# Kernel optimization log

Hardware: AMD Instinct MI355X
Metric: run time of the kernel (lower is better)

Reference implementation:

```python
import jax, jax.numpy as jnp
import numpy as np


def fps(xyz, nsamples):
    # xyz: [B, N, 3] -> [B, nsamples] furthest-point-sample indices (int32)
    def single(p):
        N = p.shape[0]
        def step(carry, _):
            dists, last = carry
            d = jnp.sum((p - p[last]) ** 2, axis=-1)
            dists = jnp.minimum(dists, d)
            return (dists, jnp.argmax(dists).astype(jnp.int32)), last
        init = (jnp.full((N,), 1e10, p.dtype), jnp.int32(0))
        _, idx = jax.lax.scan(step, init, None, length=nsamples)
        return idx
    return jax.vmap(single)(xyz)


def bn_relu(x, g, b, m, v):
    # inference BatchNorm2d folded into scale/shift, then ReLU; x: [B,C,S,N]
    s = g * jax.lax.rsqrt(v + 1e-5)
    return jax.nn.relu(x * s[None, :, None, None] + (b - m * s)[None, :, None, None])


def setup_inputs() -> dict:
    key = jax.random.key(0)
    ks = jax.random.split(key, 6)
    B, N, C, S = 8, 16384, 64, 5
    return dict(
        fg_xyz=jax.random.normal(ks[0], (B, N, 3), jnp.float32),
        fg_features=jax.random.normal(ks[1], (B, C, N), jnp.float32),
        bg_xyz=jax.random.normal(ks[2], (B, N, 3), jnp.float32),
        bg_features=jax.random.normal(ks[3], (B, C, N), jnp.float32),
        w1=jax.random.normal(ks[4], (C, 2 * C), jnp.float32) * (1.0 / np.sqrt(2 * C)),
        g1=jnp.ones((C,), jnp.float32), b1=jnp.zeros((C,), jnp.float32),
        m1=jnp.zeros((C,), jnp.float32), v1=jnp.ones((C,), jnp.float32),
        w2=jax.random.normal(ks[5], (C, C), jnp.float32) * (1.0 / np.sqrt(C)),
        g2=jnp.ones((C,), jnp.float32), b2=jnp.zeros((C,), jnp.float32),
        m2=jnp.zeros((C,), jnp.float32), v2=jnp.ones((C,), jnp.float32),
        nsamples=5,
    )


def reference(fg_xyz, fg_features, bg_xyz, bg_features,
              w1, g1, b1, m1, v1, w2, g2, b2, m2, v2, nsamples):
    B, C, N = fg_features.shape
    S = nsamples
    # D-FPS sample S background points, gather their features: [B, C, S]
    idx = fps(bg_xyz, S)
    sample_bg = jnp.take_along_axis(
        bg_features, jnp.broadcast_to(idx[:, None, :], (B, C, S)), axis=2)
    fg_exp = fg_features[:, :, None, :]                           # [B, C, 1, N]
    # candidates = [fg itself, S sampled bg feats tiled over the N fg points]
    fused_origin = jnp.concatenate(
        [fg_exp, jnp.broadcast_to(sample_bg[:, :, :, None], (B, C, S, N))], axis=2)  # [B,C,S+1,N]
    # weight-net input: fg feature concatenated with each candidate along channels
    fusion_in = jnp.concatenate(
        [jnp.broadcast_to(fg_exp, (B, C, S + 1, N)), fused_origin], axis=1)          # [B,2C,S+1,N]
    h = bn_relu(jnp.einsum('oc,bcsn->bosn', w1, fusion_in), g1, b1, m1, v1)
    w = bn_relu(jnp.einsum('oc,bcsn->bosn', w2, h), g2, b2, m2, v2)                  # [B,C,S+1,N]
    final_feats = jnp.sum(w * fused_origin, axis=2, keepdims=True)                   # [B,C,1,N]
    return fg_xyz, final_feats
```

## Files before the change

kernel.cpp:

```cpp
#include <hip/hip_runtime.h>
#include <hip/hip_bf16.h>

#define B_ 8
#define N_ 16384
#define C_ 64
#define S_ 5

typedef float v4f __attribute__((ext_vector_type(4)));
typedef __bf16 v8bf __attribute__((ext_vector_type(8)));
typedef unsigned int v4u __attribute__((ext_vector_type(4)));

static __device__ __forceinline__ unsigned short f2bf(float f) {
    unsigned int u = __float_as_uint(f);
    u += 0x7fffu + ((u >> 16) & 1u);
    return (unsigned short)(u >> 16);
}
static __device__ __forceinline__ float bf2f(unsigned short s) {
    return __uint_as_float(((unsigned int)s) << 16);
}

#define GETF(A, i) (((i) & 3) == 0 ? A[(i) >> 2].x : ((i) & 3) == 1 ? A[(i) >> 2].y \
                    : ((i) & 3) == 2 ? A[(i) >> 2].z : A[(i) >> 2].w)

__global__ __launch_bounds__(1024, 4) void prep_all(
    const float* __restrict__ bg_xyz, const float* __restrict__ bg_feat,
    const float* __restrict__ w1, const float* __restrict__ g1, const float* __restrict__ b1,
    const float* __restrict__ m1, const float* __restrict__ v1,
    const float* __restrict__ w2, const float* __restrict__ g2, const float* __restrict__ b2,
    const float* __restrict__ m2, const float* __restrict__ v2,
    const float* __restrict__ fg_xyz, float* __restrict__ out_xyz,
    float* __restrict__ bb1, float* __restrict__ bb2,
    unsigned short* __restrict__ wa_bf, unsigned short* __restrict__ wc_bf,
    unsigned short* __restrict__ w2_bf,
    float* __restrict__ sbg, float* __restrict__ ebb) {
    const int blk = blockIdx.x;
    const int t = threadIdx.x;

    if (blk >= 9) {
        const int i = (blk - 9) * 1024 + t;
        ((float4*)out_xyz)[i] = ((const float4*)fg_xyz)[i];
        return;
    }

    if (blk == 8) {
        for (int i = t; i < 64 * 64; i += 1024) {
            const int o = i >> 6, c = i & 63;
            const float s1 = g1[o] / sqrtf(v1[o] + 1e-5f);
            const float s2 = g2[o] / sqrtf(v2[o] + 1e-5f);
            const float a = s1 * w1[o * 128 + c];
            const float bbv = s1 * w1[o * 128 + 64 + c];
            wa_bf[o * 64 + c] = f2bf(a);
            wc_bf[o * 64 + c] = f2bf(a + bbv);
            w2_bf[o * 64 + c] = f2bf(s2 * w2[o * 64 + c]);
        }
        if (t < 64) {
            const float s1 = g1[t] / sqrtf(v1[t] + 1e-5f);
            const float s2 = g2[t] / sqrtf(v2[t] + 1e-5f);
            bb1[t] = b1[t] - m1[t] * s1;
            bb2[t] = b2[t] - m2[t] * s2;
        }
        return;
    }

    const int b = blk;
    const float* p = bg_xyz + (size_t)b * N_ * 3;

    float4 f4[12];
    {
        const float4* pv = (const float4*)p + t * 12;
#pragma unroll
        for (int i = 0; i < 12; ++i) f4[i] = pv[i];
    }
    float px[16], py[16], pz[16], dist[16];
#pragma unroll
    for (int k = 0; k < 16; ++k) {
        px[k] = GETF(f4, 3 * k);
        py[k] = GETF(f4, 3 * k + 1);
        pz[k] = GETF(f4, 3 * k + 2);
        dist[k] = 1e10f;
    }

    __shared__ float s_best[16];
    __shared__ int s_bidx[16];
    __shared__ int s_last;
    __shared__ int s_idx[S_];
    __shared__ float sf[S_][64];
    int last = 0;
    if (t == 0) s_idx[0] = 0;

    for (int step = 1; step < S_; ++step) {
        const float lx = p[last * 3 + 0];
        const float ly = p[last * 3 + 1];
        const float lz = p[last * 3 + 2];
        float best = -1.0f;
        int bidx = 0;
#pragma unroll
        for (int k = 0; k < 16; ++k) {
            float dx = px[k] - lx, dy = py[k] - ly, dz = pz[k] - lz;
            float d = dx * dx + dy * dy + dz * dz;
            float nd = fminf(dist[k], d);
            dist[k] = nd;
            if (nd > best) { best = nd; bidx = t * 16 + k; }
        }
#pragma unroll
        for (int off = 32; off > 0; off >>= 1) {
            float ob = __shfl_down(best, off, 64);
            int oi = __shfl_down(bidx, off, 64);
            if (ob > best || (ob == best && oi < bidx)) { best = ob; bidx = oi; }
        }
        if ((t & 63) == 0) { s_best[t >> 6] = best; s_bidx[t >> 6] = bidx; }
        __syncthreads();
        if (t == 0) {
            float bb = s_best[0];
            int bi = s_bidx[0];
#pragma unroll
            for (int w = 1; w < 16; ++w) {
                if (s_best[w] > bb || (s_best[w] == bb && s_bidx[w] < bi)) {
                    bb = s_best[w];
                    bi = s_bidx[w];
                }
            }
            s_last = bi;
            s_idx[step] = bi;
        }
        __syncthreads();
        last = s_last;
        __syncthreads();
    }

    __syncthreads();
    if (t < S_ * 64) {
        const int j = t >> 6, c = t & 63;
        sf[j][c] = bg_feat[(size_t)b * C_ * N_ + (size_t)c * N_ + s_idx[j]];
    }
    __syncthreads();
    if (t < S_ * 64) {
        const int j = t >> 6, o = t & 63;
        const float s1 = g1[o] * rsqrtf(v1[o] + 1e-5f);
        const float4* wr = (const float4*)&w1[o * 128 + 64];
        float acc = 0.f;
#pragma unroll
        for (int c4 = 0; c4 < 16; ++c4) {
            float4 wv = wr[c4];
            acc += wv.x * sf[j][c4 * 4 + 0] + wv.y * sf[j][c4 * 4 + 1] +
                   wv.z * sf[j][c4 * 4 + 2] + wv.w * sf[j][c4 * 4 + 3];
        }
        sbg[(b * S_ + j) * 64 + o] = sf[j][o];
        ebb[(b * S_ + j) * 64 + o] = s1 * acc + (b1[o] - m1[o] * s1);
    }
}

#define PITCH 72

__global__ __launch_bounds__(256, 4) void fusion_main(
    const float* __restrict__ fg_feat,
    const unsigned short* __restrict__ wa_bf, const unsigned short* __restrict__ wc_bf,
    const unsigned short* __restrict__ w2_bf,
    const float* __restrict__ bb1g, const float* __restrict__ bb2g,
    const float* __restrict__ ebbg, const float* __restrict__ sbgg,
    float* __restrict__ out) {
    __shared__ __align__(16) unsigned short Ft[2][64 * PITCH];
    __shared__ __align__(16) unsigned short Ht[64 * PITCH];
    __shared__ __align__(16) float cEbb[S_ * 64];
    __shared__ __align__(16) float cSbg[S_ * 64];
    __shared__ __align__(16) float cBb1[64];
    __shared__ __align__(16) float cBb2[64];

    const int t = threadIdx.x;
    const int b = blockIdx.y;
    const float* Fbase = fg_feat + (size_t)b * C_ * N_;
    const size_t outb = (size_t)b * C_ * N_;

    for (int i = t; i < S_ * 64; i += 256) {
        cEbb[i] = ebbg[b * (S_ * 64) + i];
        cSbg[i] = sbgg[b * (S_ * 64) + i];
    }
    if (t < 64) { cBb1[t] = bb1g[t]; cBb2[t] = bb2g[t]; }

    const int lane = t & 63;
    const int wv = t >> 6;
    const int o0 = wv * 16;
    const int m = lane & 15;
    const int q = lane >> 4;
    const int o4 = o0 + 4 * q;

    const int arow = o0 + m;
    v8bf aWa[2], aWc[2], aW2[2];
#pragma unroll
    for (int ks = 0; ks < 2; ++ks) {
        aWa[ks] = *(const v8bf*)&wa_bf[arow * 64 + ks * 32 + q * 8];
        aWc[ks] = *(const v8bf*)&wc_bf[arow * 64 + ks * 32 + q * 8];
        aW2[ks] = *(const v8bf*)&w2_bf[arow * 64 + ks * 32 + q * 8];
    }

    const int sn = t & 63;
    const int cg = (t >> 6) * 16;

    {
        const float* Fg = Fbase + (size_t)blockIdx.x * 64 + sn;
        float fr[16];
#pragma unroll
        for (int i = 0; i < 16; ++i) fr[i] = Fg[(size_t)(cg + i) * N_];
        v4u w0, w1v;
#pragma unroll
        for (int i = 0; i < 8; ++i) {
            unsigned int pk = (unsigned int)f2bf(fr[2 * i]) |
                              ((unsigned int)f2bf(fr[2 * i + 1]) << 16);
            if (i < 4) w0[i] = pk; else w1v[i - 4] = pk;
        }
        *(v4u*)&Ft[0][sn * PITCH + cg] = w0;
        *(v4u*)&Ft[0][sn * PITCH + cg + 8] = w1v;
    }
    __syncthreads();

    float fr1[16];
    {
        const float* Fg1 = Fbase + (size_t)(blockIdx.x + 128) * 64 + sn;
#pragma unroll
        for (int i = 0; i < 16; ++i) fr1[i] = Fg1[(size_t)(cg + i) * N_];
    }

    const v4f bb1r = *(const v4f*)&cBb1[o4];
    const v4f bb2r = *(const v4f*)&cBb2[o4];

    auto tile_compute = [&](const unsigned short* F, size_t obase) {
        v8bf bF[4][2];
#pragma unroll
        for (int nb = 0; nb < 4; ++nb)
#pragma unroll
            for (int ks = 0; ks < 2; ++ks)
                bF[nb][ks] = *(const v8bf*)&F[(nb * 16 + m) * PITCH + ks * 32 + q * 8];

        v4f U[4], U0[4];
#pragma unroll
        for (int nb = 0; nb < 4; ++nb) {
            v4f z = {0.f, 0.f, 0.f, 0.f};
            z = __builtin_amdgcn_mfma_f32_16x16x32_bf16(aWa[0], bF[nb][0], z, 0, 0, 0);
            U[nb] = __builtin_amdgcn_mfma_f32_16x16x32_bf16(aWa[1], bF[nb][1], z, 0, 0, 0);
            v4f z2 = {0.f, 0.f, 0.f, 0.f};
            z2 = __builtin_amdgcn_mfma_f32_16x16x32_bf16(aWc[0], bF[nb][0], z2, 0, 0, 0);
            U0[nb] = __builtin_amdgcn_mfma_f32_16x16x32_bf16(aWc[1], bF[nb][1], z2, 0, 0, 0);
        }

        v4f acc[4];
#pragma unroll
        for (int nb = 0; nb < 4; ++nb) acc[nb] = (v4f){0.f, 0.f, 0.f, 0.f};

#pragma unroll
        for (int s = 0; s < 6; ++s) {
            v4f cv = (s == 0) ? bb1r : *(const v4f*)&cEbb[(s - 1) * 64 + o4];
#pragma unroll
            for (int nb = 0; nb < 4; ++nb) {
                v4f u = (s == 0) ? U0[nb] : U[nb];
                float2 e01, e23;
                e01.x = fmaxf(u[0] + cv[0], 0.f);
                e01.y = fmaxf(u[1] + cv[1], 0.f);
                e23.x = fmaxf(u[2] + cv[2], 0.f);
                e23.y = fmaxf(u[3] + cv[3], 0.f);
                __hip_bfloat162 h01 = __float22bfloat162_rn(e01);
                __hip_bfloat162 h23 = __float22bfloat162_rn(e23);
                unsigned int lo, hi;
                __builtin_memcpy(&lo, &h01, 4);
                __builtin_memcpy(&hi, &h23, 4);
                unsigned long long vv = (unsigned long long)lo | ((unsigned long long)hi << 32);
                *(unsigned long long*)&Ht[(nb * 16 + m) * PITCH + o4] = vv;
            }
            __syncthreads();

            v4f p4[4];
#pragma unroll
            for (int nb = 0; nb < 4; ++nb) {
                v8bf h0 = *(const v8bf*)&Ht[(nb * 16 + m) * PITCH + q * 8];
                v8bf h1 = *(const v8bf*)&Ht[(nb * 16 + m) * PITCH + 32 + q * 8];
                v4f z = {0.f, 0.f, 0.f, 0.f};
                z = __builtin_amdgcn_mfma_f32_16x16x32_bf16(aW2[0], h0, z, 0, 0, 0);
                p4[nb] = __builtin_amdgcn_mfma_f32_16x16x32_bf16(aW2[1], h1, z, 0, 0, 0);
            }
            __syncthreads();

#pragma unroll
            for (int nb = 0; nb < 4; ++nb) {
                if (s == 0) {
                    unsigned long long fv =
                        *(const unsigned long long*)&F[(nb * 16 + m) * PITCH + o4];
#pragma unroll
                    for (int r = 0; r < 4; ++r) {
                        float wgt = fmaxf(p4[nb][r] + bb2r[r], 0.f);
                        acc[nb][r] += wgt * bf2f((unsigned short)(fv >> (16 * r)));
                    }
                } else {
                    const v4f sb = *(const v4f*)&cSbg[(s - 1) * 64 + o4];
#pragma unroll
                    for (int r = 0; r < 4; ++r) {
                        float wgt = fmaxf(p4[nb][r] + bb2r[r], 0.f);
                        acc[nb][r] += wgt * sb[r];
                    }
                }
            }
        }

#pragma unroll
        for (int nb = 0; nb < 4; ++nb)
#pragma unroll
            for (int r = 0; r < 4; ++r)
                out[obase + (size_t)(o4 + r) * N_ + (nb * 16 + m)] = acc[nb][r];
    };

    tile_compute(&Ft[0][0], outb + (size_t)blockIdx.x * 64);

    {
        v4u w0, w1v;
#pragma unroll
        for (int i = 0; i < 8; ++i) {
            unsigned int pk = (unsigned int)f2bf(fr1[2 * i]) |
                              ((unsigned int)f2bf(fr1[2 * i + 1]) << 16);
            if (i < 4) w0[i] = pk; else w1v[i - 4] = pk;
        }
        *(v4u*)&Ft[1][sn * PITCH + cg] = w0;
        *(v4u*)&Ft[1][sn * PITCH + cg + 8] = w1v;
    }
    __syncthreads();

    tile_compute(&Ft[1][0], outb + (size_t)(blockIdx.x + 128) * 64);
}

extern "C" void kernel_launch(void* const* d_in, const int* in_sizes, int n_in,
                              void* d_out, int out_size, void* d_ws, size_t ws_size,
                              hipStream_t stream) {
    const float* fg_xyz = (const float*)d_in[0];
    const float* fg_feat = (const float*)d_in[1];
    const float* bg_xyz = (const float*)d_in[2];
    const float* bg_feat = (const float*)d_in[3];
    const float* w1 = (const float*)d_in[4];
    const float* g1 = (const float*)d_in[5];
    const float* b1 = (const float*)d_in[6];
    const float* m1 = (const float*)d_in[7];
    const float* v1 = (const float*)d_in[8];
    const float* w2 = (const float*)d_in[9];
    const float* g2 = (const float*)d_in[10];
    const float* b2 = (const float*)d_in[11];
    const float* m2 = (const float*)d_in[12];
    const float* v2 = (const float*)d_in[13];

    float* ws = (float*)d_ws;
    float* ebb = ws;
    float* sbg = ebb + 2560;
    float* bb1 = sbg + 2560;
    float* bb2 = bb1 + 64;
    unsigned short* wa_bf = (unsigned short*)(bb2 + 64);
    unsigned short* wc_bf = wa_bf + 4096;
    unsigned short* w2_bf = wc_bf + 4096;

    float* out_feats = (float*)d_out + (size_t)B_ * N_ * 3;

    prep_all<<<105, 1024, 0, stream>>>(bg_xyz, bg_feat,
                                       w1, g1, b1, m1, v1, w2, g2, b2, m2, v2,
                                       fg_xyz, (float*)d_out,
                                       bb1, bb2, wa_bf, wc_bf, w2_bf, sbg, ebb);
    fusion_main<<<dim3(128, B_), 256, 0, stream>>>(
        fg_feat, wa_bf, wc_bf, w2_bf, bb1, bb2, ebb, sbg, out_feats);
}
```

Baseline: 198.0 us.

## Process one tile per block and double-buffer hidden tile to halve barriers

fusion_main now handles a single 64-point tile per block, launching twice as many blocks instead of looping over two tiles with a prefetched second tile. The hidden-activation LDS buffer is double-buffered by sample index, so the second barrier per sample step is gone and the W2 MFMA is fused with the accumulation. The change also drops the minimum-occupancy launch-bounds hints and cleans up the FPS point unpacking and bf16 packing. It removes half the syncthreads in the inner loop, but gives up the cross-tile global-load prefetch overlap.

```diff
diff --git a/kernel.cpp b/kernel.cpp
--- a/kernel.cpp
+++ b/kernel.cpp
@@ -18,11 +18,14 @@
 static __device__ __forceinline__ float bf2f(unsigned short s) {
     return __uint_as_float(((unsigned int)s) << 16);
 }
-
-#define GETF(A, i) (((i) & 3) == 0 ? A[(i) >> 2].x : ((i) & 3) == 1 ? A[(i) >> 2].y \
-                    : ((i) & 3) == 2 ? A[(i) >> 2].z : A[(i) >> 2].w)
-
-__global__ __launch_bounds__(1024, 4) void prep_all(
+static __device__ __forceinline__ unsigned int pk2bf(float a, float b) {
+    float2 f2; f2.x = a; f2.y = b;
+    __hip_bfloat162 h2 = __float22bfloat162_rn(f2);
+    unsigned int u; __builtin_memcpy(&u, &h2, 4);
+    return u;
+}
+
+__global__ __launch_bounds__(1024) void prep_all(
     const float* __restrict__ bg_xyz, const float* __restrict__ bg_feat,
     const float* __restrict__ w1, const float* __restrict__ g1, const float* __restrict__ b1,
     const float* __restrict__ m1, const float* __restrict__ v1,
@@ -65,19 +68,21 @@
     const int b = blk;
     const float* p = bg_xyz + (size_t)b * N_ * 3;
 
-    float4 f4[12];
+    float px[16], py[16], pz[16], dist[16];
     {
         const float4* pv = (const float4*)p + t * 12;
 #pragma unroll
-        for (int i = 0; i < 12; ++i) f4[i] = pv[i];
-    }
-    float px[16], py[16], pz[16], dist[16];
-#pragma unroll
-    for (int k = 0; k < 16; ++k) {
-        px[k] = GETF(f4, 3 * k);
-        py[k] = GETF(f4, 3 * k + 1);
-        pz[k] = GETF(f4, 3 * k + 2);
-        dist[k] = 1e10f;
+        for (int g = 0; g < 4; ++g) {
+            float4 a = pv[g * 3 + 0];
+            float4 bq = pv[g * 3 + 1];
+            float4 c = pv[g * 3 + 2];
+            px[g * 4 + 0] = a.x;  py[g * 4 + 0] = a.y;  pz[g * 4 + 0] = a.z;
+            px[g * 4 + 1] = a.w;  py[g * 4 + 1] = bq.x; pz[g * 4 + 1] = bq.y;
+            px[g * 4 + 2] = bq.z; py[g * 4 + 2] = bq.w; pz[g * 4 + 2] = c.x;
+            px[g * 4 + 3] = c.y;  py[g * 4 + 3] = c.z;  pz[g * 4 + 3] = c.w;
+            dist[g * 4 + 0] = 1e10f; dist[g * 4 + 1] = 1e10f;
+            dist[g * 4 + 2] = 1e10f; dist[g * 4 + 3] = 1e10f;
+        }
     }
 
     __shared__ float s_best[16];
@@ -152,15 +157,15 @@
 
 #define PITCH 72
 
-__global__ __launch_bounds__(256, 4) void fusion_main(
+__global__ __launch_bounds__(256) void fusion_main(
     const float* __restrict__ fg_feat,
     const unsigned short* __restrict__ wa_bf, const unsigned short* __restrict__ wc_bf,
     const unsigned short* __restrict__ w2_bf,
     const float* __restrict__ bb1g, const float* __restrict__ bb2g,
     const float* __restrict__ ebbg, const float* __restrict__ sbgg,
     float* __restrict__ out) {
-    __shared__ __align__(16) unsigned short Ft[2][64 * PITCH];
-    __shared__ __align__(16) unsigned short Ht[64 * PITCH];
+    __shared__ __align__(16) unsigned short Ft[64 * PITCH];
+    __shared__ __align__(16) unsigned short Ht[2][64 * PITCH];
     __shared__ __align__(16) float cEbb[S_ * 64];
     __shared__ __align__(16) float cSbg[S_ * 64];
     __shared__ __align__(16) float cBb1[64];
@@ -168,9 +173,24 @@
 
     const int t = threadIdx.x;
     const int b = blockIdx.y;
-    const float* Fbase = fg_feat + (size_t)b * C_ * N_;
-    const size_t outb = (size_t)b * C_ * N_;
-
+    const int n0 = blockIdx.x * 64;
+    const float* Fg = fg_feat + (size_t)b * C_ * N_ + n0;
+
+    {
+        const int n = t & 63;
+        const int cg = (t >> 6) * 16;
+        float fr[16];
+#pragma unroll
+        for (int i = 0; i < 16; ++i) fr[i] = Fg[(size_t)(cg + i) * N_ + n];
+        v4u w0, w1v;
+#pragma unroll
+        for (int i = 0; i < 8; ++i) {
+            unsigned int pk = pk2bf(fr[2 * i], fr[2 * i + 1]);
+            if (i < 4) w0[i] = pk; else w1v[i - 4] = pk;
+        }
+        *(v4u*)&Ft[n * PITCH + cg] = w0;
+        *(v4u*)&Ft[n * PITCH + cg + 8] = w1v;
+    }
     for (int i = t; i < S_ * 64; i += 256) {
         cEbb[i] = ebbg[b * (S_ * 64) + i];
         cSbg[i] = sbgg[b * (S_ * 64) + i];
@@ -193,135 +213,80 @@
         aW2[ks] = *(const v8bf*)&w2_bf[arow * 64 + ks * 32 + q * 8];
     }
 
-    const int sn = t & 63;
-    const int cg = (t >> 6) * 16;
-
-    {
-        const float* Fg = Fbase + (size_t)blockIdx.x * 64 + sn;
-        float fr[16];
-#pragma unroll
-        for (int i = 0; i < 16; ++i) fr[i] = Fg[(size_t)(cg + i) * N_];
-        v4u w0, w1v;
-#pragma unroll
-        for (int i = 0; i < 8; ++i) {
-            unsigned int pk = (unsigned int)f2bf(fr[2 * i]) |
-                              ((unsigned int)f2bf(fr[2 * i + 1]) << 16);
-            if (i < 4) w0[i] = pk; else w1v[i - 4] = pk;
-        }
-        *(v4u*)&Ft[0][sn * PITCH + cg] = w0;
-        *(v4u*)&Ft[0][sn * PITCH + cg + 8] = w1v;
-    }
     __syncthreads();
 
-    float fr1[16];
-    {
-        const float* Fg1 = Fbase + (size_t)(blockIdx.x + 128) * 64 + sn;
-#pragma unroll
-        for (int i = 0; i < 16; ++i) fr1[i] = Fg1[(size_t)(cg + i) * N_];
-    }
-
-    const v4f bb1r = *(const v4f*)&cBb1[o4];
+    v8bf bF[4][2];
+#pragma unroll
+    for (int nb = 0; nb < 4; ++nb)
+#pragma unroll
+        for (int ks = 0; ks < 2; ++ks)
+            bF[nb][ks] = *(const v8bf*)&Ft[(nb * 16 + m) * PITCH + ks * 32 + q * 8];
+
+    v4f U[4], U0[4];
+#pragma unroll
+    for (int nb = 0; nb < 4; ++nb) {
+        v4f z = {0.f, 0.f, 0.f, 0.f};
+        z = __builtin_amdgcn_mfma_f32_16x16x32_bf16(aWa[0], bF[nb][0], z, 0, 0, 0);
+        U[nb] = __builtin_amdgcn_mfma_f32_16x16x32_bf16(aWa[1], bF[nb][1], z, 0, 0, 0);
+        v4f z2 = {0.f, 0.f, 0.f, 0.f};
+        z2 = __builtin_amdgcn_mfma_f32_16x16x32_bf16(aWc[0], bF[nb][0], z2, 0, 0, 0);
+        U0[nb] = __builtin_amdgcn_mfma_f32_16x16x32_bf16(aWc[1], bF[nb][1], z2, 0, 0, 0);
+    }
+
+    v4f acc[4];
+#pragma unroll
+    for (int nb = 0; nb < 4; ++nb) acc[nb] = (v4f){0.f, 0.f, 0.f, 0.f};
+
     const v4f bb2r = *(const v4f*)&cBb2[o4];
 
-    auto tile_compute = [&](const unsigned short* F, size_t obase) {
-        v8bf bF[4][2];
-#pragma unroll
-        for (int nb = 0; nb < 4; ++nb)
-#pragma unroll
-            for (int ks = 0; ks < 2; ++ks)
-                bF[nb][ks] = *(const v8bf*)&F[(nb * 16 + m) * PITCH + ks * 32 + q * 8];
-
-        v4f U[4], U0[4];
+#pragma unroll
+    for (int s = 0; s < 6; ++s) {
+        unsigned short* h = &Ht[s & 1][0];
+        v4f cv = (s == 0) ? *(const v4f*)&cBb1[o4]
+                          : *(const v4f*)&cEbb[(s - 1) * 64 + o4];
 #pragma unroll
         for (int nb = 0; nb < 4; ++nb) {
+            v4f u = (s == 0) ? U0[nb] : U[nb];
+            unsigned int lo = pk2bf(fmaxf(u[0] + cv[0], 0.f), fmaxf(u[1] + cv[1], 0.f));
+            unsigned int hi = pk2bf(fmaxf(u[2] + cv[2], 0.f), fmaxf(u[3] + cv[3], 0.f));
+            unsigned long long vv = (unsigned long long)lo | ((unsigned long long)hi << 32);
+            *(unsigned long long*)&h[(nb * 16 + m) * PITCH + o4] = vv;
+        }
+        __syncthreads();
+
+#pragma unroll
+        for (int nb = 0; nb < 4; ++nb) {
+            v8bf h0 = *(const v8bf*)&h[(nb * 16 + m) * PITCH + q * 8];
+            v8bf h1 = *(const v8bf*)&h[(nb * 16 + m) * PITCH + 32 + q * 8];
             v4f z = {0.f, 0.f, 0.f, 0.f};
-            z = __builtin_amdgcn_mfma_f32_16x16x32_bf16(aWa[0], bF[nb][0], z, 0, 0, 0);
-            U[nb] = __builtin_amdgcn_mfma_f32_16x16x32_bf16(aWa[1], bF[nb][1], z, 0, 0, 0);
-            v4f z2 = {0.f, 0.f, 0.f, 0.f};
-            z2 = __builtin_amdgcn_mfma_f32_16x16x32_bf16(aWc[0], bF[nb][0], z2, 0, 0, 0);
-            U0[nb] = __builtin_amdgcn_mfma_f32_16x16x32_bf16(aWc[1], bF[nb][1], z2, 0, 0, 0);
-        }
-
-        v4f acc[4];
-#pragma unroll
-        for (int nb = 0; nb < 4; ++nb) acc[nb] = (v4f){0.f, 0.f, 0.f, 0.f};
-
-#pragma unroll
-        for (int s = 0; s < 6; ++s) {
-            v4f cv = (s == 0) ? bb1r : *(const v4f*)&cEbb[(s - 1) * 64 + o4];
-#pragma unroll
-            for (int nb = 0; nb < 4; ++nb) {
-                v4f u = (s == 0) ? U0[nb] : U[nb];
-                float2 e01, e23;
-                e01.x = fmaxf(u[0] + cv[0], 0.f);
-                e01.y = fmaxf(u[1] + cv[1], 0.f);
-                e23.x = fmaxf(u[2] + cv[2], 0.f);
-                e23.y = fmaxf(u[3] + cv[3], 0.f);
-                __hip_bfloat162 h01 = __float22bfloat162_rn(e01);
-                __hip_bfloat162 h23 = __float22bfloat162_rn(e23);
-                unsigned int lo, hi;
-                __builtin_memcpy(&lo, &h01, 4);
-                __builtin_memcpy(&hi, &h23, 4);
-                unsigned long long vv = (unsigned long long)lo | ((unsigned long long)hi << 32);
-                *(unsigned long long*)&Ht[(nb * 16 + m) * PITCH + o4] = vv;
-            }
-            __syncthreads();
-
-            v4f p4[4];
-#pragma unroll
-            for (int nb = 0; nb < 4; ++nb) {
-                v8bf h0 = *(const v8bf*)&Ht[(nb * 16 + m) * PITCH + q * 8];
-                v8bf h1 = *(const v8bf*)&Ht[(nb * 16 + m) * PITCH + 32 + q * 8];
-                v4f z = {0.f, 0.f, 0.f, 0.f};
-                z = __builtin_amdgcn_mfma_f32_16x16x32_bf16(aW2[0], h0, z, 0, 0, 0);
-                p4[nb] = __builtin_amdgcn_mfma_f32_16x16x32_bf16(aW2[1], h1, z, 0, 0, 0);
-            }
-            __syncthreads();
-
-#pragma unroll
-            for (int nb = 0; nb < 4; ++nb) {
-                if (s == 0) {
-                    unsigned long long fv =
-                        *(const unsigned long long*)&F[(nb * 16 + m) * PITCH + o4];
-#pragma unroll
-                    for (int r = 0; r < 4; ++r) {
-                        float wgt = fmaxf(p4[nb][r] + bb2r[r], 0.f);
-                        acc[nb][r] += wgt * bf2f((unsigned short)(fv >> (16 * r)));
-                    }
-                } else {
-                    const v4f sb = *(const v4f*)&cSbg[(s - 1) * 64 + o4];
-#pragma unroll
-                    for (int r = 0; r < 4; ++r) {
-                        float wgt = fmaxf(p4[nb][r] + bb2r[r], 0.f);
-                        acc[nb][r] += wgt * sb[r];
-                    }
+            z = __builtin_amdgcn_mfma_f32_16x16x32_bf16(aW2[0], h0, z, 0, 0, 0);
+            v4f p4 = __builtin_amdgcn_mfma_f32_16x16x32_bf16(aW2[1], h1, z, 0, 0, 0);
+
+            if (s == 0) {
+                unsigned long long fv =
+                    *(const unsigned long long*)&Ft[(nb * 16 + m) * PITCH + o4];
+#pragma unroll
+                for (int r = 0; r < 4; ++r) {
+                    float wgt = fmaxf(p4[r] + bb2r[r], 0.f);
+                    acc[nb][r] += wgt * bf2f((unsigned short)(fv >> (16 * r)));
+                }
+            } else {
+                const v4f sb = *(const v4f*)&cSbg[(s - 1) * 64 + o4];
+#pragma unroll
+                for (int r = 0; r < 4; ++r) {
+                    float wgt = fmaxf(p4[r] + bb2r[r], 0.f);
+                    acc[nb][r] += wgt * sb[r];
                 }
             }
         }
-
-#pragma unroll
-        for (int nb = 0; nb < 4; ++nb)
-#pragma unroll
-            for (int r = 0; r < 4; ++r)
-                out[obase + (size_t)(o4 + r) * N_ + (nb * 16 + m)] = acc[nb][r];
-    };
-
-    tile_compute(&Ft[0][0], outb + (size_t)blockIdx.x * 64);
-
-    {
-        v4u w0, w1v;
-#pragma unroll
-        for (int i = 0; i < 8; ++i) {
-            unsigned int pk = (unsigned int)f2bf(fr1[2 * i]) |
-                              ((unsigned int)f2bf(fr1[2 * i + 1]) << 16);
-            if (i < 4) w0[i] = pk; else w1v[i - 4] = pk;
-        }
-        *(v4u*)&Ft[1][sn * PITCH + cg] = w0;
-        *(v4u*)&Ft[1][sn * PITCH + cg + 8] = w1v;
-    }
-    __syncthreads();
-
-    tile_compute(&Ft[1][0], outb + (size_t)(blockIdx.x + 128) * 64);
+    }
+
+    const size_t outb = (size_t)b * C_ * N_ + n0;
+#pragma unroll
+    for (int nb = 0; nb < 4; ++nb)
+#pragma unroll
+        for (int r = 0; r < 4; ++r)
+            out[outb + (size_t)(o4 + r) * N_ + (nb * 16 + m)] = acc[nb][r];
 }
 
 extern "C" void kernel_launch(void* const* d_in, const int* in_sizes, int n_in,
@@ -357,6 +322,6 @@
                                        w1, g1, b1, m1, v1, w2, g2, b2, m2, v2,
                                        fg_xyz, (float*)d_out,
                                        bb1, bb2, wa_bf, wc_bf, w2_bf, sbg, ebb);
-    fusion_main<<<dim3(128, B_), 256, 0, stream>>>(
+    fusion_main<<<dim3(N_ / 64, B_), 256, 0, stream>>>(
         fg_feat, wa_bf, wc_bf, w2_bf, bb1, bb2, ebb, sbg, out_feats);
 }
```

New measurement: 164.7 us. 1.2x faster.
